# Performance work log

Hardware: AMD Instinct MI355X
Metric: run time of the kernel (lower is better)

The kernel has to match this reference:

```python
import jax, jax.numpy as jnp
import numpy as np

DIM = 512
HEADS = 8
HEAD_DIM = DIM // HEADS
WINDOW = 128
TOKEN_SELF_ATTN_VALUE = -5e4  # lucidrains local-attention constant for shared_qk self mask


def setup_inputs() -> dict:
    key = jax.random.key(0)
    k1, k2, k3, k4 = jax.random.split(key, 4)
    B, N = 4, 8192
    x = jax.random.normal(k1, (B, N, DIM), dtype=jnp.float32)
    w_qkv = jax.random.normal(k2, (3 * DIM, DIM), dtype=jnp.float32) * (DIM ** -0.5)
    w_proj = jax.random.normal(k3, (DIM, DIM), dtype=jnp.float32) * (DIM ** -0.5)
    b_proj = jax.random.normal(k4, (DIM,), dtype=jnp.float32) * 0.01
    return {"x": x, "w_qkv": w_qkv, "w_proj": w_proj, "b_proj": b_proj}


def _look_around(b):
    # b: [B,H,nw,w,D] -> [B,H,nw,2w,D] = concat(prev_window, cur_window); window 0 padded with zeros
    padded = jnp.pad(b, ((0, 0), (0, 0), (1, 0), (0, 0), (0, 0)))
    return jnp.concatenate([padded[:, :, :-1], b], axis=3)


def _local_attn(q, k, v):
    # causal sliding-window attention, window=128, look_backward=1, shared_qk
    B, H, N, D = q.shape
    w = WINDOW
    nw = N // w
    scale = D ** -0.5
    # shared_qk: l2-normalize keys (F.normalize, eps=1e-12)
    k = k / jnp.clip(jnp.linalg.norm(k, axis=-1, keepdims=True), 1e-12, None)

    bq = q.reshape(B, H, nw, w, D)
    bk = _look_around(k.reshape(B, H, nw, w, D))  # [B,H,nw,2w,D]
    bv = _look_around(v.reshape(B, H, nw, w, D))

    t = jnp.arange(N).reshape(nw, w)
    t_pad = jnp.pad(t, ((1, 0), (0, 0)), constant_values=-1)
    bq_t = t                                         # [nw, w]
    bq_k = jnp.concatenate([t_pad[:-1], t], axis=1)  # [nw, 2w]

    sim = jnp.einsum('bhwie,bhwje->bhwij', bq, bk) * scale  # [B,H,nw,w,2w]

    self_mask = bq_t[:, :, None] == bq_k[:, None, :]
    causal_mask = bq_t[:, :, None] < bq_k[:, None, :]
    pad_mask = (bq_k == -1)[:, None, :]
    mask_value = -jnp.finfo(sim.dtype).max
    sim = jnp.where(self_mask, TOKEN_SELF_ATTN_VALUE, sim)
    sim = jnp.where(causal_mask | pad_mask, mask_value, sim)

    attn = jax.nn.softmax(sim, axis=-1)  # dropout is identity in eval mode
    out = jnp.einsum('bhwij,bhwje->bhwie', attn, bv)
    return out.reshape(B, H, N, D)


def reference(x, w_qkv, w_proj, b_proj):
    B, N, C = x.shape
    qkv = x @ w_qkv.T  # [B,N,3C]
    q, k, v = jnp.split(qkv, 3, axis=-1)
    to_heads = lambda t: t.reshape(B, N, HEADS, HEAD_DIM).transpose(0, 2, 1, 3)
    out = _local_attn(to_heads(q), to_heads(k), to_heads(v))  # [B,H,N,D]
    out = out.transpose(0, 2, 1, 3).reshape(B, N, C)
    return out @ w_proj.T + b_proj
```

## Files before the change

kernel.cpp:

```cpp
#include <hip/hip_runtime.h>
#include <stdint.h>

typedef uint16_t u16;
typedef __bf16 bf16x8 __attribute__((ext_vector_type(8)));
typedef float f32x4 __attribute__((ext_vector_type(4)));
typedef uint16_t u16x4 __attribute__((ext_vector_type(4)));
typedef uint16_t u16x8 __attribute__((ext_vector_type(8)));

typedef __attribute__((address_space(1))) void as1_void;
typedef __attribute__((address_space(3))) void as3_void;

__device__ __forceinline__ float bf2f(u16 b) {
    union { uint32_t u; float f; } v; v.u = ((uint32_t)b) << 16; return v.f;
}
__device__ __forceinline__ u16 f2bf(float f) {
    union { float f; uint32_t u; } v; v.f = f;
    uint32_t u = v.u;
    u += 0x7fffu + ((u >> 16) & 1u);
    return (u16)(u >> 16);
}
__device__ __forceinline__ void gload_lds16(const u16* g, u16* l) {
    __builtin_amdgcn_global_load_lds((as1_void*)g, (as3_void*)l, 16, 0, 0);
}

__global__ __launch_bounds__(256) void cvt_w(
    const float* __restrict__ wq, u16* __restrict__ wqb,
    const float* __restrict__ wp, u16* __restrict__ wpb)
{
    const float* src; u16* dst; int base;
    const int b = blockIdx.x;
    if (b < 384) { src = wq; dst = wqb; base = b; }
    else         { src = wp; dst = wpb; base = b - 384; }
    const size_t i = ((size_t)base * 256 + threadIdx.x) * 8;
    f32x4 a = *(const f32x4*)(src + i);
    f32x4 c = *(const f32x4*)(src + i + 4);
    u16x8 o;
    o[0] = f2bf(a[0]); o[1] = f2bf(a[1]); o[2] = f2bf(a[2]); o[3] = f2bf(a[3]);
    o[4] = f2bf(c[0]); o[5] = f2bf(c[1]); o[6] = f2bf(c[2]); o[7] = f2bf(c[3]);
    *(u16x8*)(dst + i) = o;
}

template<int NT, bool NORMK>
__global__ __launch_bounds__(256, 3) void gemm_a32(
    const float* __restrict__ A, int lda,
    const u16* __restrict__ B, int ldb,
    u16* __restrict__ C, int ldc)
{
    __shared__ float lA[2][128 * 32];
    __shared__ u16   lB[2][4 * 128 * 8];

    const int tid  = threadIdx.x;
    const int lane = tid & 63;
    const int wave = tid >> 6;
    const int wr = (wave >> 1) * 64;
    const int wc = (wave & 1) * 64;
    const int cl = lane & 15;
    const int gr = lane >> 4;

    int fid = blockIdx.y * gridDim.x + blockIdx.x;
    const int nwg = gridDim.x * gridDim.y;
    fid = (fid & 7) * (nwg >> 3) + (fid >> 3);
    const int row0 = (fid / gridDim.x) * 128;
    const int col0 = (fid % gridDim.x) * 128;

    const int srowA = lane >> 3;
    const int schA  = ((lane & 7) - srowA) & 7;

    f32x4 acc[4][4] = {};

    auto STAGE = [&](int t, int d) {
        const int k0 = t * 32;
        #pragma unroll
        for (int i = 0; i < 4; ++i) {
            const int Rg = wave * 32 + i * 8;
            gload_lds16((const u16*)(A + (size_t)(row0 + Rg + srowA) * lda + k0 + schA * 4),
                        (u16*)&lA[d][Rg * 32]);
        }
        #pragma unroll
        for (int i = 0; i < 2; ++i) {
            gload_lds16(B + (size_t)(col0 + i * 64 + lane) * ldb + k0 + wave * 8,
                        &lB[d][(wave * 128 + i * 64) * 8]);
        }
    };

    STAGE(0, 0);
    STAGE(1, 1);
    #pragma unroll
    for (int t = 0; t < NT; ++t) {
        if (t < NT - 1) asm volatile("s_waitcnt vmcnt(6)" ::: "memory");
        else            asm volatile("s_waitcnt vmcnt(0)" ::: "memory");
        __builtin_amdgcn_s_barrier();
        const float* la = lA[t & 1];
        const u16*   lb = lB[t & 1];

        bf16x8 af[4], bfv[4];
        #pragma unroll
        for (int m = 0; m < 4; ++m) {
            const int ra = wr + m * 16 + cl;
            const int s0 = (gr * 2 + ra) & 7;
            const int s1 = (gr * 2 + 1 + ra) & 7;
            const f32x4 x0 = *(const f32x4*)&la[ra * 32 + s0 * 4];
            const f32x4 x1 = *(const f32x4*)&la[ra * 32 + s1 * 4];
            bf16x8 t8;
            t8[0] = (__bf16)x0[0]; t8[1] = (__bf16)x0[1];
            t8[2] = (__bf16)x0[2]; t8[3] = (__bf16)x0[3];
            t8[4] = (__bf16)x1[0]; t8[5] = (__bf16)x1[1];
            t8[6] = (__bf16)x1[2]; t8[7] = (__bf16)x1[3];
            af[m] = t8;
        }
        #pragma unroll
        for (int n = 0; n < 4; ++n) {
            const int rb = wc + n * 16 + cl;
            bfv[n] = *(const bf16x8*)&lb[(gr * 128 + rb) * 8];
        }
        __builtin_amdgcn_s_setprio(1);
        #pragma unroll
        for (int m = 0; m < 4; ++m)
            #pragma unroll
            for (int n = 0; n < 4; ++n)
                acc[m][n] = __builtin_amdgcn_mfma_f32_16x16x32_bf16(af[m], bfv[n], acc[m][n], 0, 0, 0);
        __builtin_amdgcn_s_setprio(0);
        __builtin_amdgcn_s_barrier();
        if (t + 2 < NT) STAGE(t + 2, t & 1);
    }

    if constexpr (NORMK) {
        if (col0 + wc >= 512 && col0 + wc < 1024) {
            #pragma unroll
            for (int m = 0; m < 4; ++m)
                #pragma unroll
                for (int j = 0; j < 4; ++j) {
                    float ss = 0.f;
                    #pragma unroll
                    for (int n = 0; n < 4; ++n) ss += acc[m][n][j] * acc[m][n][j];
                    ss += __shfl_xor(ss, 1);
                    ss += __shfl_xor(ss, 2);
                    ss += __shfl_xor(ss, 4);
                    ss += __shfl_xor(ss, 8);
                    const float scl = 1.f / fmaxf(sqrtf(ss), 1e-12f);
                    #pragma unroll
                    for (int n = 0; n < 4; ++n) acc[m][n][j] *= scl;
                }
        }
    }

    #pragma unroll
    for (int m = 0; m < 4; ++m) {
        const int r = row0 + wr + m * 16 + gr * 4;
        #pragma unroll
        for (int n = 0; n < 4; ++n) {
            const int c = col0 + wc + n * 16 + cl;
            #pragma unroll
            for (int j = 0; j < 4; ++j)
                C[(size_t)(r + j) * ldc + c] = f2bf(acc[m][n][j]);
        }
    }
}

template<int NT, bool C_F32, bool NORMK>
__global__ __launch_bounds__(512) void gemm256(
    const u16* __restrict__ A, int lda,
    const u16* __restrict__ B, int ldb,
    const float* __restrict__ bias,
    void* __restrict__ Cv, int ldc)
{
    __shared__ u16 lA[2][256 * 64];
    __shared__ u16 lB[2][256 * 64];

    const int tid  = threadIdx.x;
    const int lane = tid & 63;
    const int wave = tid >> 6;
    const int wm = wave >> 2;
    const int wn = wave & 3;
    const int cl = lane & 15;
    const int gr = lane >> 4;

    int fid = blockIdx.y * gridDim.x + blockIdx.x;
    const int nwg = gridDim.x * gridDim.y;
    fid = (fid & 7) * (nwg >> 3) + (fid >> 3);
    const int row0 = (fid / gridDim.x) * 256;
    const int col0 = (fid % gridDim.x) * 256;

    const int srow   = lane >> 3;
    const int schunk = ((lane & 7) - srow) & 7;

    f32x4 acc[8][4] = {};

    auto STAGE = [&](int t, int d) {
        const int k0 = t * 64;
        #pragma unroll
        for (int i = 0; i < 4; ++i) {
            const int Rg = wave * 32 + i * 8;
            gload_lds16(A + (size_t)(row0 + Rg + srow) * lda + k0 + schunk * 8,
                        &lA[d][Rg * 64]);
            gload_lds16(B + (size_t)(col0 + Rg + srow) * ldb + k0 + schunk * 8,
                        &lB[d][Rg * 64]);
        }
    };

    auto COMPUTE = [&](int d) {
        const u16* la = lA[d];
        const u16* lb = lB[d];
        bf16x8 bfrag[2][4];
        #pragma unroll
        for (int kk = 0; kk < 2; ++kk)
            #pragma unroll
            for (int n = 0; n < 4; ++n) {
                const int rb = wn * 64 + n * 16 + cl;
                bfrag[kk][n] = *(const bf16x8*)(lb + rb * 64 + (((kk * 4 + gr + rb) & 7) * 8));
            }
        __builtin_amdgcn_s_setprio(1);
        #pragma unroll
        for (int m = 0; m < 8; ++m) {
            const int ra = wm * 128 + m * 16 + cl;
            const bf16x8 a0 = *(const bf16x8*)(la + ra * 64 + (((gr + ra) & 7) * 8));
            const bf16x8 a1 = *(const bf16x8*)(la + ra * 64 + (((4 + gr + ra) & 7) * 8));
            #pragma unroll
            for (int n = 0; n < 4; ++n)
                acc[m][n] = __builtin_amdgcn_mfma_f32_16x16x32_bf16(a0, bfrag[0][n], acc[m][n], 0, 0, 0);
            #pragma unroll
            for (int n = 0; n < 4; ++n)
                acc[m][n] = __builtin_amdgcn_mfma_f32_16x16x32_bf16(a1, bfrag[1][n], acc[m][n], 0, 0, 0);
        }
        __builtin_amdgcn_s_setprio(0);
    };

    STAGE(0, 0);
    STAGE(1, 1);
    #pragma unroll
    for (int t = 0; t < NT; ++t) {
        if (t < NT - 1) asm volatile("s_waitcnt vmcnt(8)" ::: "memory");
        else            asm volatile("s_waitcnt vmcnt(0)" ::: "memory");
        __builtin_amdgcn_s_barrier();
        COMPUTE(t & 1);
        __builtin_amdgcn_s_barrier();
        if (t + 2 < NT) STAGE(t + 2, t & 1);
    }

    if constexpr (NORMK) {
        if (col0 + wn * 64 >= 512 && col0 + wn * 64 < 1024) {
            #pragma unroll
            for (int m = 0; m < 8; ++m)
                #pragma unroll
                for (int j = 0; j < 4; ++j) {
                    float ss = 0.f;
                    #pragma unroll
                    for (int n = 0; n < 4; ++n) ss += acc[m][n][j] * acc[m][n][j];
                    ss += __shfl_xor(ss, 1);
                    ss += __shfl_xor(ss, 2);
                    ss += __shfl_xor(ss, 4);
                    ss += __shfl_xor(ss, 8);
                    const float scl = 1.f / fmaxf(sqrtf(ss), 1e-12f);
                    #pragma unroll
                    for (int n = 0; n < 4; ++n) acc[m][n][j] *= scl;
                }
        }
    }

    #pragma unroll
    for (int m = 0; m < 8; ++m) {
        const int r = row0 + wm * 128 + m * 16 + gr * 4;
        #pragma unroll
        for (int n = 0; n < 4; ++n) {
            const int c = col0 + wn * 64 + n * 16 + cl;
            const float bv = bias ? bias[c] : 0.f;
            #pragma unroll
            for (int j = 0; j < 4; ++j) {
                const float val = acc[m][n][j] + bv;
                if constexpr (C_F32) ((float*)Cv)[(size_t)(r + j) * ldc + c] = val;
                else                 ((u16*)Cv)[(size_t)(r + j) * ldc + c] = f2bf(val);
            }
        }
    }
}

template<bool A_F32, bool C_F32, bool NORMK>
__global__ __launch_bounds__(256) void gemm_bt_f32(
    const void* __restrict__ Av, int lda,
    const float* __restrict__ B, int ldb,
    const float* __restrict__ bias,
    void* __restrict__ Cv, int ldc,
    int K)
{
    __shared__ u16 lA[128 * 32];
    __shared__ u16 lB[128 * 32];

    const int tid  = threadIdx.x;
    const int lane = tid & 63;
    const int wave = tid >> 6;
    const int wr   = (wave >> 1) * 64;
    const int wc   = (wave & 1) * 64;
    const int row0 = blockIdx.y * 128;
    const int col0 = blockIdx.x * 128;

    f32x4 acc[4][4] = {};

    for (int k0 = 0; k0 < K; k0 += 32) {
        #pragma unroll
        for (int i = 0; i < 4; ++i) {
            const int idx = i * 256 + tid;
            const int r = idx >> 3;
            const int p = (idx & 7) * 4;
            u16x4 a4, b4;
            if constexpr (A_F32) {
                const float* Af = (const float*)Av;
                f32x4 va = *(const f32x4*)(Af + (size_t)(row0 + r) * lda + k0 + p);
                a4[0] = f2bf(va[0]); a4[1] = f2bf(va[1]); a4[2] = f2bf(va[2]); a4[3] = f2bf(va[3]);
            } else {
                const u16* Ab = (const u16*)Av;
                a4 = *(const u16x4*)(Ab + (size_t)(row0 + r) * lda + k0 + p);
            }
            {
                f32x4 vb = *(const f32x4*)(B + (size_t)(col0 + r) * ldb + k0 + p);
                b4[0] = f2bf(vb[0]); b4[1] = f2bf(vb[1]); b4[2] = f2bf(vb[2]); b4[3] = f2bf(vb[3]);
            }
            *(u16x4*)&lA[r * 32 + p] = a4;
            *(u16x4*)&lB[r * 32 + p] = b4;
        }
        __syncthreads();

        bf16x8 af[4], bfv[4];
        #pragma unroll
        for (int m = 0; m < 4; ++m)
            af[m] = *(const bf16x8*)(lA + (wr + m * 16 + (lane & 15)) * 32 + (lane >> 4) * 8);
        #pragma unroll
        for (int n = 0; n < 4; ++n)
            bfv[n] = *(const bf16x8*)(lB + (wc + n * 16 + (lane & 15)) * 32 + (lane >> 4) * 8);
        #pragma unroll
        for (int m = 0; m < 4; ++m)
            #pragma unroll
            for (int n = 0; n < 4; ++n)
                acc[m][n] = __builtin_amdgcn_mfma_f32_16x16x32_bf16(af[m], bfv[n], acc[m][n], 0, 0, 0);
        __syncthreads();
    }

    if constexpr (NORMK) {
        if (col0 >= 512 && col0 < 1024) {
            #pragma unroll
            for (int m = 0; m < 4; ++m)
                #pragma unroll
                for (int j = 0; j < 4; ++j) {
                    float ss = 0.f;
                    #pragma unroll
                    for (int n = 0; n < 4; ++n) ss += acc[m][n][j] * acc[m][n][j];
                    ss += __shfl_xor(ss, 1);
                    ss += __shfl_xor(ss, 2);
                    ss += __shfl_xor(ss, 4);
                    ss += __shfl_xor(ss, 8);
                    const float scl = 1.f / fmaxf(sqrtf(ss), 1e-12f);
                    #pragma unroll
                    for (int n = 0; n < 4; ++n) acc[m][n][j] *= scl;
                }
        }
    }

    #pragma unroll
    for (int m = 0; m < 4; ++m) {
        const int r = row0 + wr + m * 16 + ((lane >> 4) << 2);
        #pragma unroll
        for (int n = 0; n < 4; ++n) {
            const int c = col0 + wc + n * 16 + (lane & 15);
            const float bv = bias ? bias[c] : 0.f;
            #pragma unroll
            for (int j = 0; j < 4; ++j) {
                const float val = acc[m][n][j] + bv;
                if constexpr (C_F32) ((float*)Cv)[(size_t)(r + j) * ldc + c] = val;
                else                 ((u16*)Cv)[(size_t)(r + j) * ldc + c] = f2bf(val);
            }
        }
    }
}

__global__ __launch_bounds__(512, 4) void attn_kernel(const u16* qkv, u16* o)
{
    constexpr int CC = 1536;
    constexpr int NTOK = 8192;
    constexpr int KP = 72;
    constexpr int VP = 136;
    constexpr int PP = 136;
    __shared__ u16 kn[128 * KP];
    __shared__ u16 vT[64 * VP];
    __shared__ u16 Pl[128 * PP];

    const int tid  = threadIdx.x;
    const int lane = tid & 63;
    const int wave = tid >> 6;
    const int cl = lane & 15;
    const int gr = lane >> 4;

    int blk = blockIdx.x;
    blk = (blk & 7) * (gridDim.x >> 3) + (blk >> 3);

    const int iw  = blk & 63;
    const int h   = (blk >> 6) & 7;
    const int b   = blk >> 9;

    const int tq0 = iw * 128;
    const size_t rowbase = (size_t)b * NTOK;
    const u16* qbase = qkv + rowbase * CC + h * 64;
    const u16* kbase = qbase + 512;
    const u16* vbase = qbase + 1024;

    const int wrow = wave * 16;
    bf16x8 qf[2];
    #pragma unroll
    for (int kk = 0; kk < 2; ++kk)
        qf[kk] = *(const bf16x8*)(qbase + (size_t)(tq0 + wrow + cl) * CC + kk * 32 + gr * 8);

    f32x4 oacc[4] = {};
    float m_run[4] = {-3.0e38f, -3.0e38f, -3.0e38f, -3.0e38f};
    float l_run[4] = {0.f, 0.f, 0.f, 0.f};

    for (int c = 0; c < 2; ++c) {
        const int tkc = tq0 - 128 + c * 128;

        #pragma unroll
        for (int p = 0; p < 2; ++p) {
            const int id = tid + p * 512;
            const int row = id >> 3, dc = id & 7;
            u16x8 v8 = {};
            if (tkc >= 0) v8 = *(const u16x8*)(kbase + (size_t)(tkc + row) * CC + dc * 8);
            *(u16x8*)&kn[row * KP + dc * 8] = v8;
        }
        #pragma unroll
        for (int p = 0; p < 2; ++p) {
            const int id = tid + p * 512;
            const int key = id & 127, dc = id >> 7;
            u16x8 v8 = {};
            if (tkc >= 0) v8 = *(const u16x8*)(vbase + (size_t)(tkc + key) * CC + dc * 8);
            #pragma unroll
            for (int e = 0; e < 8; ++e) vT[(dc * 8 + e) * VP + key] = v8[e];
        }
        __syncthreads();

        f32x4 s[8] = {};
        #pragma unroll
        for (int n = 0; n < 8; ++n)
            #pragma unroll
            for (int kk = 0; kk < 2; ++kk) {
                const bf16x8 kf = *(const bf16x8*)&kn[(n * 16 + cl) * KP + kk * 32 + gr * 8];
                s[n] = __builtin_amdgcn_mfma_f32_16x16x32_bf16(qf[kk], kf, s[n], 0, 0, 0);
            }

        float pmax[4] = {-3.0e38f, -3.0e38f, -3.0e38f, -3.0e38f};
        #pragma unroll
        for (int n = 0; n < 8; ++n) {
            const int tkk = tkc + n * 16 + cl;
            const bool pad = tkk < 0;
            #pragma unroll
            for (int j = 0; j < 4; ++j) {
                const int tq = tq0 + wrow + gr * 4 + j;
                float sv = s[n][j] * 0.125f;
                const int rel = tkk - tq;
                sv = (rel == 0) ? -5.0e4f : sv;
                sv = (rel > 0 || pad) ? -6.0e4f : sv;
                s[n][j] = sv;
                pmax[j] = fmaxf(pmax[j], sv);
            }
        }
        float cold[4];
        #pragma unroll
        for (int j = 0; j < 4; ++j) {
            pmax[j] = fmaxf(pmax[j], __shfl_xor(pmax[j], 1));
            pmax[j] = fmaxf(pmax[j], __shfl_xor(pmax[j], 2));
            pmax[j] = fmaxf(pmax[j], __shfl_xor(pmax[j], 4));
            pmax[j] = fmaxf(pmax[j], __shfl_xor(pmax[j], 8));
            const float mn = fmaxf(m_run[j], pmax[j]);
            cold[j] = __expf(m_run[j] - mn);
            m_run[j] = mn;
            l_run[j] *= cold[j];
        }
        #pragma unroll
        for (int n = 0; n < 8; ++n)
            #pragma unroll
            for (int j = 0; j < 4; ++j) {
                const float p = __expf(s[n][j] - m_run[j]);
                s[n][j] = p;
                l_run[j] += p;
            }
        #pragma unroll
        for (int n = 0; n < 4; ++n) {
            f32x4 t = oacc[n];
            t[0] *= cold[0]; t[1] *= cold[1]; t[2] *= cold[2]; t[3] *= cold[3];
            oacc[n] = t;
        }
        #pragma unroll
        for (int n = 0; n < 8; ++n)
            #pragma unroll
            for (int j = 0; j < 4; ++j)
                Pl[(wrow + gr * 4 + j) * PP + n * 16 + cl] = f2bf(s[n][j]);
        __syncthreads();

        #pragma unroll
        for (int kk = 0; kk < 4; ++kk) {
            const bf16x8 pa = *(const bf16x8*)&Pl[(wrow + cl) * PP + kk * 32 + gr * 8];
            #pragma unroll
            for (int n = 0; n < 4; ++n) {
                const bf16x8 vb = *(const bf16x8*)&vT[(n * 16 + cl) * VP + kk * 32 + gr * 8];
                oacc[n] = __builtin_amdgcn_mfma_f32_16x16x32_bf16(pa, vb, oacc[n], 0, 0, 0);
            }
        }
        __syncthreads();
    }

    float inv[4];
    #pragma unroll
    for (int j = 0; j < 4; ++j) {
        l_run[j] += __shfl_xor(l_run[j], 1);
        l_run[j] += __shfl_xor(l_run[j], 2);
        l_run[j] += __shfl_xor(l_run[j], 4);
        l_run[j] += __shfl_xor(l_run[j], 8);
        inv[j] = 1.f / l_run[j];
    }
    u16* obase = o + rowbase * CC + h * 64;
    const int r0 = tq0 + wrow + gr * 4;
    #pragma unroll
    for (int n = 0; n < 4; ++n) {
        const int d = n * 16 + cl;
        #pragma unroll
        for (int j = 0; j < 4; ++j)
            obase[(size_t)(r0 + j) * CC + d] = f2bf(oacc[n][j] * inv[j]);
    }
}

extern "C" void kernel_launch(void* const* d_in, const int* in_sizes, int n_in,
                              void* d_out, int out_size, void* d_ws, size_t ws_size,
                              hipStream_t stream)
{
    (void)in_sizes; (void)n_in; (void)out_size;
    const float* x      = (const float*)d_in[0];
    const float* w_qkv  = (const float*)d_in[1];
    const float* w_proj = (const float*)d_in[2];
    const float* b_proj = (const float*)d_in[3];
    float* out = (float*)d_out;

    const int BN = 4 * 8192;
    const size_t qkv_b = (size_t)BN * 1536 * 2;
    const size_t wq_b  = (size_t)1536 * 512 * 2;
    const size_t wp_b  = (size_t)512 * 512 * 2;

    uint8_t* p = (uint8_t*)d_ws;
    u16* qkv = (u16*)p;

    if (ws_size >= qkv_b + wq_b + wp_b) {
        u16* wqb = (u16*)(p + qkv_b);
        u16* wpb = (u16*)(p + qkv_b + wq_b);
        cvt_w<<<512, 256, 0, stream>>>(w_qkv, wqb, w_proj, wpb);
        gemm_a32<16, true><<<dim3(12, 256), 256, 0, stream>>>(
            x, 512, wqb, 512, qkv, 1536);
        attn_kernel<<<dim3(4 * 8 * 64), 512, 0, stream>>>(qkv, qkv);
        gemm256<8, true, false><<<dim3(2, 128), 512, 0, stream>>>(
            qkv, 1536, wpb, 512, b_proj, out, 512);
    } else {
        gemm_bt_f32<true, false, true><<<dim3(12, BN / 128), 256, 0, stream>>>(
            x, 512, w_qkv, 512, nullptr, qkv, 1536, 512);
        attn_kernel<<<dim3(4 * 8 * 64), 512, 0, stream>>>(qkv, qkv);
        gemm_bt_f32<false, true, false><<<dim3(4, BN / 128), 256, 0, stream>>>(
            qkv, 1536, w_proj, 512, b_proj, out, 512, 512);
    }
}
```

Baseline: 192.2 us.

## Pre-convert x to bf16 and deepen QKV GEMM pipeline to four LDS stages

Adds a conversion pass that turns the fp32 activations into bf16 alongside the weights, so the QKV GEMM loads bf16 A tiles instead of converting fp32 in registers after each LDS read. The GEMM now uses a 4-buffer LDS ring with three tiles in flight, prefetches the next iteration's fragments into registers during the MFMAs, and needs only one barrier per iteration. This removes the in-loop fp32→bf16 conversion and halves the A-tile LDS traffic. In exchange it adds an extra read and write of x through a 32 MB bf16 workspace, plus a larger workspace requirement, and occupancy drops from 3 to 2 blocks per CU.

```diff
diff --git a/kernel.cpp b/kernel.cpp
--- a/kernel.cpp
+++ b/kernel.cpp
@@ -23,31 +23,37 @@
     __builtin_amdgcn_global_load_lds((as1_void*)g, (as3_void*)l, 16, 0, 0);
 }
 
-__global__ __launch_bounds__(256) void cvt_w(
+__global__ __launch_bounds__(256) void cvt3(
+    const float* __restrict__ x,  u16* __restrict__ xb,
     const float* __restrict__ wq, u16* __restrict__ wqb,
     const float* __restrict__ wp, u16* __restrict__ wpb)
 {
-    const float* src; u16* dst; int base;
+    const float* src; u16* dst; int base, nb;
     const int b = blockIdx.x;
-    if (b < 384) { src = wq; dst = wqb; base = b; }
-    else         { src = wp; dst = wpb; base = b - 384; }
-    const size_t i = ((size_t)base * 256 + threadIdx.x) * 8;
-    f32x4 a = *(const f32x4*)(src + i);
-    f32x4 c = *(const f32x4*)(src + i + 4);
-    u16x8 o;
-    o[0] = f2bf(a[0]); o[1] = f2bf(a[1]); o[2] = f2bf(a[2]); o[3] = f2bf(a[3]);
-    o[4] = f2bf(c[0]); o[5] = f2bf(c[1]); o[6] = f2bf(c[2]); o[7] = f2bf(c[3]);
-    *(u16x8*)(dst + i) = o;
+    if (b < 1024)      { src = x;  dst = xb;  base = b;        nb = 1024; }
+    else if (b < 1072) { src = wq; dst = wqb; base = b - 1024; nb = 48;   }
+    else               { src = wp; dst = wpb; base = b - 1072; nb = 16;   }
+    size_t i = ((size_t)base * 256 + threadIdx.x) * 8;
+    const size_t stride = (size_t)nb * 256 * 8;
+    #pragma unroll
+    for (int it = 0; it < 8; ++it, i += stride) {
+        f32x4 a = *(const f32x4*)(src + i);
+        f32x4 c = *(const f32x4*)(src + i + 4);
+        u16x8 o;
+        o[0] = f2bf(a[0]); o[1] = f2bf(a[1]); o[2] = f2bf(a[2]); o[3] = f2bf(a[3]);
+        o[4] = f2bf(c[0]); o[5] = f2bf(c[1]); o[6] = f2bf(c[2]); o[7] = f2bf(c[3]);
+        *(u16x8*)(dst + i) = o;
+    }
 }
 
 template<int NT, bool NORMK>
-__global__ __launch_bounds__(256, 3) void gemm_a32(
-    const float* __restrict__ A, int lda,
+__global__ __launch_bounds__(256, 2) void gemm_pipe(
+    const u16* __restrict__ A, int lda,
     const u16* __restrict__ B, int ldb,
     u16* __restrict__ C, int ldc)
 {
-    __shared__ float lA[2][128 * 32];
-    __shared__ u16   lB[2][4 * 128 * 8];
+    __shared__ u16 lA[4][128 * 32];
+    __shared__ u16 lB[4][128 * 32];
 
     const int tid  = threadIdx.x;
     const int lane = tid & 63;
@@ -63,56 +69,44 @@
     const int row0 = (fid / gridDim.x) * 128;
     const int col0 = (fid % gridDim.x) * 128;
 
-    const int srowA = lane >> 3;
-    const int schA  = ((lane & 7) - srowA) & 7;
-
     f32x4 acc[4][4] = {};
 
     auto STAGE = [&](int t, int d) {
         const int k0 = t * 32;
         #pragma unroll
-        for (int i = 0; i < 4; ++i) {
-            const int Rg = wave * 32 + i * 8;
-            gload_lds16((const u16*)(A + (size_t)(row0 + Rg + srowA) * lda + k0 + schA * 4),
-                        (u16*)&lA[d][Rg * 32]);
-        }
-        #pragma unroll
         for (int i = 0; i < 2; ++i) {
-            gload_lds16(B + (size_t)(col0 + i * 64 + lane) * ldb + k0 + wave * 8,
-                        &lB[d][(wave * 128 + i * 64) * 8]);
+            const int id  = i * 256 + tid;
+            const int row = id >> 2;
+            const int sch = ((id & 3) - ((row >> 1) & 3)) & 3;
+            gload_lds16(A + (size_t)(row0 + row) * lda + k0 + sch * 8, &lA[d][id * 8]);
+            gload_lds16(B + (size_t)(col0 + row) * ldb + k0 + sch * 8, &lB[d][id * 8]);
         }
     };
 
-    STAGE(0, 0);
-    STAGE(1, 1);
-    #pragma unroll
-    for (int t = 0; t < NT; ++t) {
-        if (t < NT - 1) asm volatile("s_waitcnt vmcnt(6)" ::: "memory");
-        else            asm volatile("s_waitcnt vmcnt(0)" ::: "memory");
-        __builtin_amdgcn_s_barrier();
-        const float* la = lA[t & 1];
-        const u16*   lb = lB[t & 1];
-
-        bf16x8 af[4], bfv[4];
+    bf16x8 af[4], bfv[4];
+    auto READS = [&](int t) {
+        const u16* la = lA[t & 3];
+        const u16* lb = lB[t & 3];
         #pragma unroll
         for (int m = 0; m < 4; ++m) {
             const int ra = wr + m * 16 + cl;
-            const int s0 = (gr * 2 + ra) & 7;
-            const int s1 = (gr * 2 + 1 + ra) & 7;
-            const f32x4 x0 = *(const f32x4*)&la[ra * 32 + s0 * 4];
-            const f32x4 x1 = *(const f32x4*)&la[ra * 32 + s1 * 4];
-            bf16x8 t8;
-            t8[0] = (__bf16)x0[0]; t8[1] = (__bf16)x0[1];
-            t8[2] = (__bf16)x0[2]; t8[3] = (__bf16)x0[3];
-            t8[4] = (__bf16)x1[0]; t8[5] = (__bf16)x1[1];
-            t8[6] = (__bf16)x1[2]; t8[7] = (__bf16)x1[3];
-            af[m] = t8;
+            af[m] = *(const bf16x8*)&la[ra * 32 + ((gr + (ra >> 1)) & 3) * 8];
         }
         #pragma unroll
         for (int n = 0; n < 4; ++n) {
             const int rb = wc + n * 16 + cl;
-            bfv[n] = *(const bf16x8*)&lb[(gr * 128 + rb) * 8];
-        }
+            bfv[n] = *(const bf16x8*)&lb[rb * 32 + ((gr + (rb >> 1)) & 3) * 8];
+        }
+    };
+
+    STAGE(0, 0); STAGE(1, 1); STAGE(2, 2);
+    asm volatile("s_waitcnt vmcnt(4)" ::: "memory");
+    __builtin_amdgcn_s_barrier();
+    READS(0);
+
+    #pragma unroll
+    for (int t = 0; t < NT; ++t) {
+        if (t + 3 < NT) STAGE(t + 3, (t + 3) & 3);
         __builtin_amdgcn_s_setprio(1);
         #pragma unroll
         for (int m = 0; m < 4; ++m)
@@ -120,8 +114,13 @@
             for (int n = 0; n < 4; ++n)
                 acc[m][n] = __builtin_amdgcn_mfma_f32_16x16x32_bf16(af[m], bfv[n], acc[m][n], 0, 0, 0);
         __builtin_amdgcn_s_setprio(0);
-        __builtin_amdgcn_s_barrier();
-        if (t + 2 < NT) STAGE(t + 2, t & 1);
+        if (t + 1 < NT) READS(t + 1);
+        if (t < NT - 1) {
+            asm volatile("s_waitcnt lgkmcnt(0)" ::: "memory");
+            if (t + 3 < NT) asm volatile("s_waitcnt vmcnt(4)" ::: "memory");
+            else            asm volatile("s_waitcnt vmcnt(0)" ::: "memory");
+            __builtin_amdgcn_s_barrier();
+        }
     }
 
     if constexpr (NORMK) {
@@ -536,18 +535,20 @@
 
     const int BN = 4 * 8192;
     const size_t qkv_b = (size_t)BN * 1536 * 2;
+    const size_t xb_b  = (size_t)BN * 512 * 2;
     const size_t wq_b  = (size_t)1536 * 512 * 2;
     const size_t wp_b  = (size_t)512 * 512 * 2;
 
     uint8_t* p = (uint8_t*)d_ws;
     u16* qkv = (u16*)p;
 
-    if (ws_size >= qkv_b + wq_b + wp_b) {
-        u16* wqb = (u16*)(p + qkv_b);
-        u16* wpb = (u16*)(p + qkv_b + wq_b);
-        cvt_w<<<512, 256, 0, stream>>>(w_qkv, wqb, w_proj, wpb);
-        gemm_a32<16, true><<<dim3(12, 256), 256, 0, stream>>>(
-            x, 512, wqb, 512, qkv, 1536);
+    if (ws_size >= qkv_b + xb_b + wq_b + wp_b) {
+        u16* xb  = (u16*)(p + qkv_b);
+        u16* wqb = (u16*)(p + qkv_b + xb_b);
+        u16* wpb = (u16*)(p + qkv_b + xb_b + wq_b);
+        cvt3<<<1088, 256, 0, stream>>>(x, xb, w_qkv, wqb, w_proj, wpb);
+        gemm_pipe<16, true><<<dim3(12, 256), 256, 0, stream>>>(
+            xb, 512, wqb, 512, qkv, 1536);
         attn_kernel<<<dim3(4 * 8 * 64), 512, 0, stream>>>(qkv, qkv);
         gemm256<8, true, false><<<dim3(2, 128), 512, 0, stream>>>(
             qkv, 1536, wpb, 512, b_proj, out, 512);
```

Result: faster. 176.9 us, median of 2 (-7.9%).
